# Performance work log

Hardware: AMD Instinct MI355X
Metric: run time of the kernel (lower is better)

## Reference

```python
import jax, jax.numpy as jnp
import numpy as np

D_MODEL = 1024
NUM_HEADS = 16
DEPTH = D_MODEL // NUM_HEADS


def setup_inputs() -> dict:
    key = jax.random.key(0)
    ks = jax.random.split(key, 11)
    B, S, D = 2, 2048, D_MODEL
    s = 1.0 / np.sqrt(D)
    inp = {
        'x': jax.random.normal(ks[0], (B, S, D), jnp.float32),
        'pH': jax.random.normal(ks[1], (B, 1, 1), jnp.float32),
        'Wq': jax.random.normal(ks[2], (D, D), jnp.float32) * s,
        'bq': jnp.zeros((D,), jnp.float32),
        'Wk': jax.random.normal(ks[3], (D, D), jnp.float32) * s,
        'bk': jnp.zeros((D,), jnp.float32),
        'Wv': jax.random.normal(ks[4], (D, D), jnp.float32) * s,
        'bv': jnp.zeros((D,), jnp.float32),
        'Wo': jax.random.normal(ks[5], (D, D), jnp.float32) * s,
        'bo': jnp.zeros((D,), jnp.float32),
    }
    return inp


def reference(x, pH, Wq, bq, Wk, bk, Wv, bv, Wo, bo):
    B, S, D = x.shape
    H, dh = NUM_HEADS, DEPTH
    # QKV projections -> [B, H, S, dh]
    def proj(W, b):
        return (x @ W + b).reshape(B, S, H, dh).transpose(0, 2, 1, 3)
    q = proj(Wq, bq)
    k = proj(Wk, bk)
    v = proj(Wv, bv)
    # scores [B, H, S, S] with additive per-sample pH bias broadcast over heads/positions
    scores = jnp.einsum('bhqd,bhkd->bhqk', q, k) / jnp.sqrt(jnp.asarray(dh, x.dtype))
    scores = scores + pH[:, :, :, None]  # [B,1,1,1] broadcasts to [B,H,S,S]
    attn = jax.nn.softmax(scores, axis=-1)
    out = jnp.einsum('bhqk,bhkd->bhqd', attn, v)  # [B,H,S,dh]
    out = out.transpose(0, 2, 1, 3).reshape(B, S, D)
    return out @ Wo + bo  # dropout p=0.0 -> identity
```

## Files before the change

### kernel.cpp

```cpp
#include <hip/hip_runtime.h>
#include <hip/hip_bf16.h>
#include <math.h>

#define BATCH 2
#define SEQ   2048
#define DMODEL 1024
#define NHEADS 16
#define DHEAD 64
#define MROWS (BATCH*SEQ)

typedef __attribute__((ext_vector_type(8))) short bf16x8;
typedef __attribute__((ext_vector_type(4))) short bf16x4;
typedef __attribute__((ext_vector_type(4))) float f32x4;

__device__ __forceinline__ short f2bf(float f) {
    union { float f; unsigned u; } c; c.f = f;
    unsigned r = (c.u + 0x7fffu + ((c.u >> 16) & 1u)) >> 16;
    return (short)r;
}
__device__ __forceinline__ float bf2f(short h) {
    union { unsigned u; float f; } c; c.u = ((unsigned)(unsigned short)h) << 16;
    return c.f;
}

__device__ __forceinline__ void async_ld16(const void* g, void* l) {
    __builtin_amdgcn_global_load_lds(
        (const __attribute__((address_space(1))) unsigned*)g,
        (__attribute__((address_space(3))) unsigned*)l, 16, 0, 0);
}

__global__ __launch_bounds__(256) void prep(
    const float* __restrict__ x, short* __restrict__ xhi,
    const float* __restrict__ W0, const float* __restrict__ W1,
    const float* __restrict__ W2, const float* __restrict__ W3,
    short* __restrict__ oqkv, short* __restrict__ oo)
{
    __shared__ float T[64][65];
    const int tid = threadIdx.x;
    if (blockIdx.x < 2048) {
        const int i = blockIdx.x * 256 + tid;
        const float4* p = (const float4*)x + (size_t)i * 2;
        float4 a = p[0], b = p[1];
        float v[8] = {a.x, a.y, a.z, a.w, b.x, b.y, b.z, b.w};
        bf16x8 H;
        #pragma unroll
        for (int j = 0; j < 8; ++j) H[j] = f2bf(v[j]);
        *((bf16x8*)xhi + i) = H;
        return;
    }
    const int bi = blockIdx.x - 2048;
    const int z = bi >> 8;
    const int t = bi & 255;
    const float* W = (z == 0) ? W0 : (z == 1) ? W1 : (z == 2) ? W2 : W3;
    short* out = (z < 3) ? (oqkv + (size_t)z * 1024 * 1024) : oo;
    const int n0 = (t & 15) * 64, k0 = (t >> 4) * 64;
    #pragma unroll
    for (int i = 0; i < 16; ++i) {
        const int idx = tid + i * 256;
        const int r = idx >> 6, c = idx & 63;
        T[r][c] = W[(size_t)(k0 + r) * DMODEL + n0 + c];
    }
    __syncthreads();
    #pragma unroll
    for (int i = 0; i < 4; ++i) {
        const int idx = tid + i * 256;
        const int r = idx >> 4, g = idx & 15;
        bf16x4 H;
        #pragma unroll
        for (int j = 0; j < 4; ++j)
            H[j] = f2bf(T[g * 4 + j][r]);
        *(bf16x4*)(out + (size_t)(n0 + r) * DMODEL + k0 + g * 4) = H;
    }
}

__global__ __launch_bounds__(256) void qkv_gemm(
    const short* __restrict__ Ahi, const short* __restrict__ Bthi,
    const float* __restrict__ b0, const float* __restrict__ b1, const float* __restrict__ b2,
    short* __restrict__ oqh, short* __restrict__ okh, short* __restrict__ ovh,
    float qscale)
{
    __shared__ short Ah[64 * 64], Bh[128 * 64];

    const int tid  = threadIdx.x;
    const int lane = tid & 63;
    const int w    = tid >> 6;
    const int quad = lane >> 4;
    const int l15  = lane & 15;
    const int wr   = w >> 1, wc = w & 1;
    const int m0   = blockIdx.y * 64;
    const int n0   = blockIdx.x * 128;
    const int K    = DMODEL;

    f32x4 acc[2][4] = {};

    for (int k0 = 0; k0 < K; k0 += 64) {
        __syncthreads();
        #pragma unroll
        for (int j = 0; j < 6; ++j) {
            const int base = w * 384 + j * 64;
            const int c = base + lane;
            if (base < 512) {
                const int row = c >> 3, pos = (c & 7) ^ (row & 7);
                async_ld16(Ahi + (size_t)(m0 + row) * K + k0 + pos * 8, Ah + base * 8);
            } else {
                const int cb = c - 512;
                const int row = cb >> 3, pos = (cb & 7) ^ (row & 7);
                async_ld16(Bthi + (size_t)(n0 + row) * K + k0 + pos * 8, Bh + (base - 512) * 8);
            }
        }
        __syncthreads();

        #pragma unroll
        for (int s = 0; s < 2; ++s) {
            bf16x8 afh[2], bfh[4];
            #pragma unroll
            for (int mi = 0; mi < 2; ++mi) {
                const int row = wr * 32 + mi * 16 + l15;
                const int pos = (s * 4 + quad) ^ (row & 7);
                afh[mi] = *(const bf16x8*)(Ah + row * 64 + pos * 8);
            }
            #pragma unroll
            for (int ni = 0; ni < 4; ++ni) {
                const int row = wc * 64 + ni * 16 + l15;
                const int pos = (s * 4 + quad) ^ (row & 7);
                bfh[ni] = *(const bf16x8*)(Bh + row * 64 + pos * 8);
            }
            #pragma unroll
            for (int mi = 0; mi < 2; ++mi)
                #pragma unroll
                for (int ni = 0; ni < 4; ++ni)
                    acc[mi][ni] = __builtin_amdgcn_mfma_f32_16x16x32_bf16(
                        afh[mi], bfh[ni], acc[mi][ni], 0, 0, 0);
        }
    }

    const int nbase = n0 + wc * 64;
    const int which = nbase >> 10;
    const int hh = (nbase & 1023) >> 6;
    const int mb = m0 + wr * 32;
    const int b = mb >> 11, sbase = mb & (SEQ - 1);
    __syncthreads();
    short* scr = (w < 2) ? (Ah + w * 2048) : (Bh + (w - 2) * 2048);

    if (which < 2) {
        const float* bias = which ? b1 : b0;
        short* dstp = which ? okh : oqh;
        const float scl = which ? 1.0f : qscale;
        #pragma unroll
        for (int mi = 0; mi < 2; ++mi)
            #pragma unroll
            for (int ni = 0; ni < 4; ++ni)
                #pragma unroll
                for (int r = 0; r < 4; ++r) {
                    const int sloc = mi * 16 + quad * 4 + r;
                    const int dloc = ni * 16 + l15;
                    const int nn = (nbase + ni * 16 + l15) & 1023;
                    scr[sloc * 64 + (((dloc >> 3) ^ (sloc & 7)) * 8) + (dloc & 7)] =
                        f2bf((acc[mi][ni][r] + bias[nn]) * scl);
                }
        #pragma unroll
        for (int i = 0; i < 4; ++i) {
            const int sloc = i * 8 + (lane >> 3);
            const int cph = (lane & 7) ^ (sloc & 7);
            bf16x8 row = *(const bf16x8*)(scr + sloc * 64 + cph * 8);
            const int dloc = (lane & 7) * 8;
            *(bf16x8*)(dstp + ((size_t)(b * NHEADS + hh) * SEQ + sbase + sloc) * DHEAD + dloc) = row;
        }
    } else {
        #pragma unroll
        for (int mi = 0; mi < 2; ++mi)
            #pragma unroll
            for (int ni = 0; ni < 4; ++ni)
                #pragma unroll
                for (int r = 0; r < 4; ++r) {
                    const int sloc = mi * 16 + quad * 4 + r;
                    const int dloc = ni * 16 + l15;
                    const int nn = (nbase + ni * 16 + l15) & 1023;
                    scr[dloc * 32 + (((sloc >> 3) ^ (dloc & 3)) * 8) + (sloc & 7)] =
                        f2bf(acc[mi][ni][r] + b2[nn]);
                }
        #pragma unroll
        for (int i = 0; i < 4; ++i) {
            const int dloc = i * 16 + (lane >> 2);
            const int cph = (lane & 3) ^ (dloc & 3);
            bf16x8 row = *(const bf16x8*)(scr + dloc * 32 + cph * 8);
            const int sg = sbase + (lane & 3) * 8;
            *(bf16x8*)(ovh + ((size_t)(b * NHEADS + hh) * DHEAD + dloc) * SEQ + sg) = row;
        }
    }
}

__global__ __launch_bounds__(256) void ogemm(
    const short* __restrict__ Ahi, const short* __restrict__ Bthi,
    const float* __restrict__ b0, float* __restrict__ outf)
{
    __shared__ short Ah[64 * 64], Bh[64 * 64];

    const int tid  = threadIdx.x;
    const int lane = tid & 63;
    const int w    = tid >> 6;
    const int quad = lane >> 4;
    const int l15  = lane & 15;
    const int wr   = w >> 1, wc = w & 1;
    const int m0   = blockIdx.y * 64;
    const int n0   = blockIdx.x * 64;
    const int K    = DMODEL;

    f32x4 acc[2][2] = {};

    for (int k0 = 0; k0 < K; k0 += 64) {
        __syncthreads();
        #pragma unroll
        for (int j = 0; j < 4; ++j) {
            const int base = w * 256 + j * 64;
            const int c = base + lane;
            if (base < 512) {
                const int row = c >> 3, pos = (c & 7) ^ (row & 7);
                async_ld16(Ahi + (size_t)(m0 + row) * K + k0 + pos * 8, Ah + base * 8);
            } else {
                const int cb = c - 512;
                const int row = cb >> 3, pos = (cb & 7) ^ (row & 7);
                async_ld16(Bthi + (size_t)(n0 + row) * K + k0 + pos * 8, Bh + (base - 512) * 8);
            }
        }
        __syncthreads();

        #pragma unroll
        for (int s = 0; s < 2; ++s) {
            bf16x8 afh[2], bfh[2];
            #pragma unroll
            for (int mi = 0; mi < 2; ++mi) {
                const int row = wr * 32 + mi * 16 + l15;
                const int pos = (s * 4 + quad) ^ (row & 7);
                afh[mi] = *(const bf16x8*)(Ah + row * 64 + pos * 8);
            }
            #pragma unroll
            for (int ni = 0; ni < 2; ++ni) {
                const int row = wc * 32 + ni * 16 + l15;
                const int pos = (s * 4 + quad) ^ (row & 7);
                bfh[ni] = *(const bf16x8*)(Bh + row * 64 + pos * 8);
            }
            #pragma unroll
            for (int mi = 0; mi < 2; ++mi)
                #pragma unroll
                for (int ni = 0; ni < 2; ++ni)
                    acc[mi][ni] = __builtin_amdgcn_mfma_f32_16x16x32_bf16(
                        afh[mi], bfh[ni], acc[mi][ni], 0, 0, 0);
        }
    }

    #pragma unroll
    for (int mi = 0; mi < 2; ++mi)
        #pragma unroll
        for (int ni = 0; ni < 2; ++ni)
            #pragma unroll
            for (int r = 0; r < 4; ++r) {
                const int m = m0 + wr * 32 + mi * 16 + quad * 4 + r;
                const int nn = n0 + wc * 32 + ni * 16 + l15;
                outf[(size_t)m * DMODEL + nn] = acc[mi][ni][r] + b0[nn];
            }
}

__global__ __launch_bounds__(256) void attn_mfma(
    const short* __restrict__ Qh_g, const short* __restrict__ Kh_g,
    const short* __restrict__ Vth_g,
    short* __restrict__ op0, float* __restrict__ l0g)
{
    __shared__ short Ksh[4096];
    __shared__ short Vsh[4096];
    __shared__ short Ph[4][1024];

    const int tid  = threadIdx.x;
    const int lane = tid & 63;
    const int w    = tid >> 6;
    const int quad = lane >> 4;
    const int l15  = lane & 15;

    const int bh    = blockIdx.x & 31;
    const int sk    = (blockIdx.x >> 5) & 3;
    const int qtile = blockIdx.x >> 7;
    const int q0    = qtile * 128 + w * 32;
    const size_t kvb = (size_t)bh * SEQ * DHEAD;

    bf16x8 ones;
    #pragma unroll
    for (int j = 0; j < 8; ++j) ones[j] = (short)0x3f80;

    bf16x8 qA[2], qB[2];
    {
        const size_t qrA = kvb + (size_t)(q0 + l15) * DHEAD;
        const size_t qrB = kvb + (size_t)(q0 + 16 + l15) * DHEAD;
        qA[0] = *(const bf16x8*)(Qh_g + qrA + quad * 8);
        qA[1] = *(const bf16x8*)(Qh_g + qrA + 32 + quad * 8);
        qB[0] = *(const bf16x8*)(Qh_g + qrB + quad * 8);
        qB[1] = *(const bf16x8*)(Qh_g + qrB + 32 + quad * 8);
    }

    const bool isv = (w >= 2);
    short* dst = isv ? Vsh : Ksh;
    int srow[4], spos[4];
    #pragma unroll
    for (int j = 0; j < 4; ++j) {
        const int c = (w & 1) * 256 + j * 64 + lane;
        srow[j] = c >> 3;
        spos[j] = (c & 7) ^ (srow[j] & 7);
    }

    f32x4 oA[4] = {}, oB[4] = {};
    f32x4 lAv = {}, lBv = {};

    const int kb0 = sk * (SEQ / 4), kb1 = kb0 + SEQ / 4;
    for (int kb = kb0; kb < kb1; kb += 64) {
        __syncthreads();
        {
            const short* src = isv ? (Vth_g + kvb + kb) : (Kh_g + kvb + (size_t)kb * DHEAD);
            #pragma unroll
            for (int j = 0; j < 4; ++j) {
                const short* g = src + (isv ? ((size_t)srow[j] * SEQ + spos[j] * 8)
                                            : ((size_t)srow[j] * DHEAD + spos[j] * 8));
                async_ld16(g, dst + ((w & 1) * 256 + j * 64) * 8);
            }
        }
        __syncthreads();

        uint2 pkB[4];
        #pragma unroll
        for (int mf = 0; mf < 4; ++mf) {
            const int row = mf * 16 + l15;
            const int sw = row & 7;
            bf16x8 kh0 = *(const bf16x8*)(Ksh + row * 64 + ((quad ^ sw) * 8));
            bf16x8 kh1 = *(const bf16x8*)(Ksh + row * 64 + (((4 + quad) ^ sw) * 8));
            f32x4 cA = {}, cB = {};
            cA = __builtin_amdgcn_mfma_f32_16x16x32_bf16(kh0, qA[0], cA, 0, 0, 0);
            cA = __builtin_amdgcn_mfma_f32_16x16x32_bf16(kh1, qA[1], cA, 0, 0, 0);
            cB = __builtin_amdgcn_mfma_f32_16x16x32_bf16(kh0, qB[0], cB, 0, 0, 0);
            cB = __builtin_amdgcn_mfma_f32_16x16x32_bf16(kh1, qB[1], cB, 0, 0, 0);

            unsigned uA[4], uB[4];
            #pragma unroll
            for (int r = 0; r < 4; ++r) {
                union { float f; unsigned u; } p;
                p.f = __builtin_amdgcn_exp2f(cA[r]);
                uA[r] = p.u;
                p.f = __builtin_amdgcn_exp2f(cB[r]);
                uB[r] = p.u;
            }
            uint2 pkA;
            pkA.x = __builtin_amdgcn_perm(uA[1], uA[0], 0x07060302u);
            pkA.y = __builtin_amdgcn_perm(uA[3], uA[2], 0x07060302u);
            pkB[mf].x = __builtin_amdgcn_perm(uB[1], uB[0], 0x07060302u);
            pkB[mf].y = __builtin_amdgcn_perm(uB[3], uB[2], 0x07060302u);
            const int pc = (mf * 2 + (quad >> 1)) ^ (l15 & 7);
            const int paddr = l15 * 64 + pc * 8 + (quad & 1) * 4;
            *(uint2*)(&Ph[w][paddr]) = pkA;
        }

        const int psw = l15 & 7;
        bf16x8 pA0 = *(const bf16x8*)(&Ph[w][l15 * 64 + ((quad ^ psw) * 8)]);
        bf16x8 pA1 = *(const bf16x8*)(&Ph[w][l15 * 64 + (((4 + quad) ^ psw) * 8)]);

        lAv = __builtin_amdgcn_mfma_f32_16x16x32_bf16(pA0, ones, lAv, 0, 0, 0);
        lAv = __builtin_amdgcn_mfma_f32_16x16x32_bf16(pA1, ones, lAv, 0, 0, 0);
        #pragma unroll
        for (int nf = 0; nf < 4; ++nf) {
            const int row = nf * 16 + l15;
            const int sw = row & 7;
            bf16x8 vh0 = *(const bf16x8*)(Vsh + row * 64 + ((quad ^ sw) * 8));
            bf16x8 vh1 = *(const bf16x8*)(Vsh + row * 64 + (((4 + quad) ^ sw) * 8));
            f32x4 cA = oA[nf];
            cA = __builtin_amdgcn_mfma_f32_16x16x32_bf16(pA0, vh0, cA, 0, 0, 0);
            cA = __builtin_amdgcn_mfma_f32_16x16x32_bf16(pA1, vh1, cA, 0, 0, 0);
            oA[nf] = cA;
        }

        #pragma unroll
        for (int mf = 0; mf < 4; ++mf) {
            const int pc = (mf * 2 + (quad >> 1)) ^ (l15 & 7);
            const int paddr = l15 * 64 + pc * 8 + (quad & 1) * 4;
            *(uint2*)(&Ph[w][paddr]) = pkB[mf];
        }
        bf16x8 pB0 = *(const bf16x8*)(&Ph[w][l15 * 64 + ((quad ^ psw) * 8)]);
        bf16x8 pB1 = *(const bf16x8*)(&Ph[w][l15 * 64 + (((4 + quad) ^ psw) * 8)]);

        lBv = __builtin_amdgcn_mfma_f32_16x16x32_bf16(pB0, ones, lBv, 0, 0, 0);
        lBv = __builtin_amdgcn_mfma_f32_16x16x32_bf16(pB1, ones, lBv, 0, 0, 0);
        #pragma unroll
        for (int nf = 0; nf < 4; ++nf) {
            const int row = nf * 16 + l15;
            const int sw = row & 7;
            bf16x8 vh0 = *(const bf16x8*)(Vsh + row * 64 + ((quad ^ sw) * 8));
            bf16x8 vh1 = *(const bf16x8*)(Vsh + row * 64 + (((4 + quad) ^ sw) * 8));
            f32x4 cB = oB[nf];
            cB = __builtin_amdgcn_mfma_f32_16x16x32_bf16(pB0, vh0, cB, 0, 0, 0);
            cB = __builtin_amdgcn_mfma_f32_16x16x32_bf16(pB1, vh1, cB, 0, 0, 0);
            oB[nf] = cB;
        }
    }

    short* op = op0 + (size_t)sk * 4194304;
    float* lg = l0g + sk * 65536;
    const int b = bh >> 4, hh = bh & 15;
    #pragma unroll
    for (int r = 0; r < 4; ++r) {
        const int qa = q0 + quad * 4 + r;
        if (l15 == 0) {
            lg[bh * SEQ + qa] = lAv[r];
            lg[bh * SEQ + qa + 16] = lBv[r];
        }
    }
    #pragma unroll
    for (int nf = 0; nf < 4; ++nf) {
        #pragma unroll
        for (int r = 0; r < 4; ++r) {
            const int qa = q0 + quad * 4 + r;
            const int d = nf * 16 + l15;
            op[(size_t)(b * SEQ + qa) * DMODEL + hh * DHEAD + d] = f2bf(oA[nf][r]);
            op[(size_t)(b * SEQ + qa + 16) * DMODEL + hh * DHEAD + d] = f2bf(oB[nf][r]);
        }
    }
}

__global__ __launch_bounds__(256) void combine_o(
    const short* __restrict__ op0, const float* __restrict__ l0g,
    short* __restrict__ aoh)
{
    const int i = blockIdx.x * 256 + threadIdx.x;
    const size_t e = (size_t)i * 8;
    const int qg = (int)(e >> 10);
    const int col = (int)(e & 1023);
    const int b = qg >> 11;
    const int q = qg & (SEQ - 1);
    const int bhq = (b * NHEADS + (col >> 6)) * SEQ + q;
    const float inv = 1.0f / (l0g[bhq] + l0g[bhq + 65536] +
                              l0g[bhq + 2 * 65536] + l0g[bhq + 3 * 65536]);

    bf16x8 a0 = *((const bf16x8*)op0 + i);
    bf16x8 a1 = *((const bf16x8*)(op0 + 4194304) + i);
    bf16x8 a2 = *((const bf16x8*)(op0 + 2 * 4194304) + i);
    bf16x8 a3 = *((const bf16x8*)(op0 + 3 * 4194304) + i);
    bf16x8 H;
    #pragma unroll
    for (int j = 0; j < 8; ++j)
        H[j] = f2bf((bf2f(a0[j]) + bf2f(a1[j]) + bf2f(a2[j]) + bf2f(a3[j])) * inv);
    *((bf16x8*)aoh + i) = H;
}

extern "C" void kernel_launch(void* const* d_in, const int* in_sizes, int n_in,
                              void* d_out, int out_size, void* d_ws, size_t ws_size,
                              hipStream_t stream) {
    const float* x  = (const float*)d_in[0];
    const float* Wq = (const float*)d_in[2];
    const float* bq = (const float*)d_in[3];
    const float* Wk = (const float*)d_in[4];
    const float* bk = (const float*)d_in[5];
    const float* Wv = (const float*)d_in[6];
    const float* bv = (const float*)d_in[7];
    const float* Wo = (const float*)d_in[8];
    const float* bo = (const float*)d_in[9];
    float* out = (float*)d_out;

    char* ws = (char*)d_ws;
    const size_t MB = 1024 * 1024;
    short* qh  = (short*)(ws + 0 * MB);
    short* kh  = (short*)(ws + 16 * MB);
    short* vth = (short*)(ws + 32 * MB);
    short* aoh = (short*)(ws + 48 * MB);
    short* op0 = (short*)(ws + 56 * MB);
    short* xhi = (short*)(ws + 64 * MB);
    short* wqkv_hi = (short*)(ws + 80 * MB);
    float* l0g = (float*)(ws + 88 * MB);
    short* wto_hi  = (short*)(ws + 92 * MB);

    dim3 blk(256);

    hipLaunchKernelGGL(prep, dim3(2048 + 1024), blk, 0, stream,
                       x, xhi, Wq, Wk, Wv, Wo, wqkv_hi, wto_hi);

    const float qscale = 0.125f * 1.44269504088896f;
    hipLaunchKernelGGL(qkv_gemm, dim3(3072 / 128, MROWS / 64), blk, 0, stream,
                       xhi, wqkv_hi, bq, bk, bv, qh, kh, vth, qscale);

    hipLaunchKernelGGL(attn_mfma, dim3(BATCH * NHEADS * (SEQ / 128) * 4), blk, 0, stream,
                       qh, kh, vth, op0, l0g);

    hipLaunchKernelGGL(combine_o, dim3(MROWS * DMODEL / 8 / 256), blk, 0, stream,
                       op0, l0g, aoh);

    hipLaunchKernelGGL(ogemm, dim3(1024 / 64, MROWS / 64), blk, 0, stream,
                       aoh, wto_hi, bo, out);
}
```

Baseline: 194.5 us.

## Register-prefetch K/V tiles and transpose P via permlane swaps instead of LDS

The attention kernel now prefetches the next K/V tile into registers during compute, then stores it to LDS at the top of the next iteration, replacing the synchronous global_load_lds path. The P matrix round-trip through shared memory is replaced with v_permlane32/16_swap register shuffles, removing the Ph buffer. The A and B PV MFMAs are also interleaved in one loop, so each V fragment is read from LDS once. This cuts LDS traffic and exposed load latency but raises register pressure, and its correctness depends on the permlane layout matching the MFMA operand layout.

```diff
diff --git a/kernel.cpp b/kernel.cpp
--- a/kernel.cpp
+++ b/kernel.cpp
@@ -27,6 +27,17 @@
     __builtin_amdgcn_global_load_lds(
         (const __attribute__((address_space(1))) unsigned*)g,
         (__attribute__((address_space(3))) unsigned*)l, 16, 0, 0);
+}
+
+__device__ __forceinline__ void pl32swap(unsigned &a, unsigned &b) {
+    asm("v_permlane32_swap_b32 %0, %1" : "+v"(a), "+v"(b));
+}
+__device__ __forceinline__ void pl16swap(unsigned &a, unsigned &b) {
+    asm("v_permlane16_swap_b32 %0, %1" : "+v"(a), "+v"(b));
+}
+__device__ __forceinline__ bf16x8 mk8(unsigned a, unsigned b, unsigned c, unsigned d) {
+    union { unsigned u[4]; bf16x8 h; } t;
+    t.u[0] = a; t.u[1] = b; t.u[2] = c; t.u[3] = d; return t.h;
 }
 
 __global__ __launch_bounds__(256) void prep(
@@ -268,7 +279,6 @@
 {
     __shared__ short Ksh[4096];
     __shared__ short Vsh[4096];
-    __shared__ short Ph[4][1024];
 
     const int tid  = threadIdx.x;
     const int lane = tid & 63;
@@ -298,32 +308,39 @@
 
     const bool isv = (w >= 2);
     short* dst = isv ? Vsh : Ksh;
-    int srow[4], spos[4];
+    int goff[4]; short* ldst[4];
     #pragma unroll
     for (int j = 0; j < 4; ++j) {
         const int c = (w & 1) * 256 + j * 64 + lane;
-        srow[j] = c >> 3;
-        spos[j] = (c & 7) ^ (srow[j] & 7);
-    }
+        const int row = c >> 3, pos = (c & 7) ^ (row & 7);
+        goff[j] = isv ? (row * SEQ + pos * 8) : (row * DHEAD + pos * 8);
+        ldst[j] = dst + (size_t)c * 8;
+    }
+
+    const int kb0 = sk * (SEQ / 4), kb1 = kb0 + SEQ / 4;
+    const int step = isv ? 64 : 64 * DHEAD;
+    const short* src = isv ? (Vth_g + kvb + kb0) : (Kh_g + kvb + (size_t)kb0 * DHEAD);
 
     f32x4 oA[4] = {}, oB[4] = {};
     f32x4 lAv = {}, lBv = {};
 
-    const int kb0 = sk * (SEQ / 4), kb1 = kb0 + SEQ / 4;
+    bf16x8 stg[4];
+    #pragma unroll
+    for (int j = 0; j < 4; ++j) stg[j] = *(const bf16x8*)(src + goff[j]);
+    src += step;
+
     for (int kb = kb0; kb < kb1; kb += 64) {
         __syncthreads();
-        {
-            const short* src = isv ? (Vth_g + kvb + kb) : (Kh_g + kvb + (size_t)kb * DHEAD);
-            #pragma unroll
-            for (int j = 0; j < 4; ++j) {
-                const short* g = src + (isv ? ((size_t)srow[j] * SEQ + spos[j] * 8)
-                                            : ((size_t)srow[j] * DHEAD + spos[j] * 8));
-                async_ld16(g, dst + ((w & 1) * 256 + j * 64) * 8);
-            }
-        }
-        __syncthreads();
-
-        uint2 pkB[4];
+        #pragma unroll
+        for (int j = 0; j < 4; ++j) *(bf16x8*)ldst[j] = stg[j];
+        __syncthreads();
+        if (kb + 64 < kb1) {
+            #pragma unroll
+            for (int j = 0; j < 4; ++j) stg[j] = *(const bf16x8*)(src + goff[j]);
+            src += step;
+        }
+
+        unsigned pa[8], pb[8];
         #pragma unroll
         for (int mf = 0; mf < 4; ++mf) {
             const int row = mf * 16 + l15;
@@ -345,54 +362,42 @@
                 p.f = __builtin_amdgcn_exp2f(cB[r]);
                 uB[r] = p.u;
             }
-            uint2 pkA;
-            pkA.x = __builtin_amdgcn_perm(uA[1], uA[0], 0x07060302u);
-            pkA.y = __builtin_amdgcn_perm(uA[3], uA[2], 0x07060302u);
-            pkB[mf].x = __builtin_amdgcn_perm(uB[1], uB[0], 0x07060302u);
-            pkB[mf].y = __builtin_amdgcn_perm(uB[3], uB[2], 0x07060302u);
-            const int pc = (mf * 2 + (quad >> 1)) ^ (l15 & 7);
-            const int paddr = l15 * 64 + pc * 8 + (quad & 1) * 4;
-            *(uint2*)(&Ph[w][paddr]) = pkA;
-        }
-
-        const int psw = l15 & 7;
-        bf16x8 pA0 = *(const bf16x8*)(&Ph[w][l15 * 64 + ((quad ^ psw) * 8)]);
-        bf16x8 pA1 = *(const bf16x8*)(&Ph[w][l15 * 64 + (((4 + quad) ^ psw) * 8)]);
+            pa[mf * 2]     = __builtin_amdgcn_perm(uA[1], uA[0], 0x07060302u);
+            pa[mf * 2 + 1] = __builtin_amdgcn_perm(uA[3], uA[2], 0x07060302u);
+            pb[mf * 2]     = __builtin_amdgcn_perm(uB[1], uB[0], 0x07060302u);
+            pb[mf * 2 + 1] = __builtin_amdgcn_perm(uB[3], uB[2], 0x07060302u);
+        }
+
+        pl32swap(pa[0], pa[2]); pl32swap(pa[1], pa[3]);
+        pl32swap(pa[4], pa[6]); pl32swap(pa[5], pa[7]);
+        pl16swap(pa[0], pa[2]); pl16swap(pa[1], pa[3]);
+        pl16swap(pa[4], pa[6]); pl16swap(pa[5], pa[7]);
+        pl32swap(pb[0], pb[2]); pl32swap(pb[1], pb[3]);
+        pl32swap(pb[4], pb[6]); pl32swap(pb[5], pb[7]);
+        pl16swap(pb[0], pb[2]); pl16swap(pb[1], pb[3]);
+        pl16swap(pb[4], pb[6]); pl16swap(pb[5], pb[7]);
+        bf16x8 pA0 = mk8(pa[0], pa[1], pa[2], pa[3]);
+        bf16x8 pA1 = mk8(pa[4], pa[5], pa[6], pa[7]);
+        bf16x8 pB0 = mk8(pb[0], pb[1], pb[2], pb[3]);
+        bf16x8 pB1 = mk8(pb[4], pb[5], pb[6], pb[7]);
 
         lAv = __builtin_amdgcn_mfma_f32_16x16x32_bf16(pA0, ones, lAv, 0, 0, 0);
         lAv = __builtin_amdgcn_mfma_f32_16x16x32_bf16(pA1, ones, lAv, 0, 0, 0);
+        lBv = __builtin_amdgcn_mfma_f32_16x16x32_bf16(pB0, ones, lBv, 0, 0, 0);
+        lBv = __builtin_amdgcn_mfma_f32_16x16x32_bf16(pB1, ones, lBv, 0, 0, 0);
+
         #pragma unroll
         for (int nf = 0; nf < 4; ++nf) {
             const int row = nf * 16 + l15;
             const int sw = row & 7;
             bf16x8 vh0 = *(const bf16x8*)(Vsh + row * 64 + ((quad ^ sw) * 8));
             bf16x8 vh1 = *(const bf16x8*)(Vsh + row * 64 + (((4 + quad) ^ sw) * 8));
-            f32x4 cA = oA[nf];
+            f32x4 cA = oA[nf], cB = oB[nf];
             cA = __builtin_amdgcn_mfma_f32_16x16x32_bf16(pA0, vh0, cA, 0, 0, 0);
             cA = __builtin_amdgcn_mfma_f32_16x16x32_bf16(pA1, vh1, cA, 0, 0, 0);
-            oA[nf] = cA;
-        }
-
-        #pragma unroll
-        for (int mf = 0; mf < 4; ++mf) {
-            const int pc = (mf * 2 + (quad >> 1)) ^ (l15 & 7);
-            const int paddr = l15 * 64 + pc * 8 + (quad & 1) * 4;
-            *(uint2*)(&Ph[w][paddr]) = pkB[mf];
-        }
-        bf16x8 pB0 = *(const bf16x8*)(&Ph[w][l15 * 64 + ((quad ^ psw) * 8)]);
-        bf16x8 pB1 = *(const bf16x8*)(&Ph[w][l15 * 64 + (((4 + quad) ^ psw) * 8)]);
-
-        lBv = __builtin_amdgcn_mfma_f32_16x16x32_bf16(pB0, ones, lBv, 0, 0, 0);
-        lBv = __builtin_amdgcn_mfma_f32_16x16x32_bf16(pB1, ones, lBv, 0, 0, 0);
-        #pragma unroll
-        for (int nf = 0; nf < 4; ++nf) {
-            const int row = nf * 16 + l15;
-            const int sw = row & 7;
-            bf16x8 vh0 = *(const bf16x8*)(Vsh + row * 64 + ((quad ^ sw) * 8));
-            bf16x8 vh1 = *(const bf16x8*)(Vsh + row * 64 + (((4 + quad) ^ sw) * 8));
-            f32x4 cB = oB[nf];
             cB = __builtin_amdgcn_mfma_f32_16x16x32_bf16(pB0, vh0, cB, 0, 0, 0);
             cB = __builtin_amdgcn_mfma_f32_16x16x32_bf16(pB1, vh1, cB, 0, 0, 0);
+            oA[nf] = cA;
             oB[nf] = cB;
         }
     }
```

Measured after the change: 194.9 us. No clear change (+0.2%).
